# Kernel tuning notes

Measured on AMD Instinct MI355X. Metric: run time of the kernel, lower is better.

## Reference

```python
import jax, jax.numpy as jnp
import numpy as np

HEADS = 4
DIM_HEAD = 32
DIM = 512
HIDDEN = HEADS * DIM_HEAD  # 128


def setup_inputs() -> dict:
    key = jax.random.key(0)
    k1, k2, k3, k4 = jax.random.split(key, 4)
    b, l = 8, 8192
    x = jax.random.normal(k1, (b, DIM, l), dtype=jnp.float32)
    # Conv1d kernel_size=1 weights stored as [out_ch, in_ch] (squeeze kernel dim)
    w_qkv = jax.random.normal(k2, (HIDDEN * 3, DIM), dtype=jnp.float32) * (1.0 / np.sqrt(DIM))
    w_out = jax.random.normal(k3, (DIM, HIDDEN), dtype=jnp.float32) * (1.0 / np.sqrt(HIDDEN))
    b_out = jax.random.normal(k4, (DIM,), dtype=jnp.float32) * 0.01
    return {"x": x, "w_qkv": w_qkv, "w_out": w_out, "b_out": b_out}


def reference(x, w_qkv, w_out, b_out):
    b, c, l = x.shape
    # 1x1 conv == channel matmul: [b, 3*hidden, l]
    qkv = jnp.einsum('oc,bcl->bol', w_qkv, x)
    # split into q, k, v each [b, heads, dim_head, l]
    qkv = qkv.reshape(b, 3, HEADS, DIM_HEAD, l)
    q, k, v = qkv[:, 0], qkv[:, 1], qkv[:, 2]
    k = jax.nn.softmax(k, axis=-1)  # softmax over sequence positions
    # context: [b, h, d, e] (small dim_head x dim_head per head)
    context = jnp.einsum('bhdn,bhen->bhde', k, v)
    out = jnp.einsum('bhde,bhdn->bhen', context, q)  # [b, h, e, l]
    out = out.reshape(b, HIDDEN, l)
    return jnp.einsum('oc,bcl->bol', w_out, out) + b_out[None, :, None]
```

## Files before the change

### kernel.cpp

```cpp
#include <hip/hip_runtime.h>
#include <math.h>
#include <stdint.h>


#define L_LEN 8192L
#define DIMC 512

typedef short bf16x8 __attribute__((ext_vector_type(8)));
typedef float f32x4 __attribute__((ext_vector_type(4)));

__device__ __forceinline__ unsigned short f2bf(float f) {
    uint32_t u = __float_as_uint(f);
    u += 0x7FFFu + ((u >> 16) & 1u);
    return (unsigned short)(u >> 16);
}
__device__ __forceinline__ void unpack8(uint4 u, float* f) {
    f[0] = __uint_as_float(u.x << 16); f[1] = __uint_as_float(u.x & 0xFFFF0000u);
    f[2] = __uint_as_float(u.y << 16); f[3] = __uint_as_float(u.y & 0xFFFF0000u);
    f[4] = __uint_as_float(u.z << 16); f[5] = __uint_as_float(u.z & 0xFFFF0000u);
    f[6] = __uint_as_float(u.w << 16); f[7] = __uint_as_float(u.w & 0xFFFF0000u);
}

#define GLOAD_LDS16(g, l) __builtin_amdgcn_global_load_lds( \
    (const __attribute__((address_space(1))) uint32_t*)(g), \
    (__attribute__((address_space(3))) uint32_t*)(l), 16, 0, 0)

__global__ __launch_bounds__(256)
void misc_kernel(const float* __restrict__ w, unsigned short* __restrict__ wb,
                 float* __restrict__ zbase)
{
    int idx = blockIdx.x * 256 + threadIdx.x;
    if (idx < 196608) wb[idx] = f2bf(w[idx]);
    else {
        int z = idx - 196608;
        if (z < 33792) zbase[z] = 0.0f;
    }
}

__global__ __launch_bounds__(256)
void xpose_cvt_kernel(const float* __restrict__ x, unsigned short* __restrict__ xb)
{
    const int b  = blockIdx.z;
    const int c0 = blockIdx.y * 64;
    const int l0 = blockIdx.x * 64;
    const float* xp = x + (long)b * DIMC * L_LEN;
    unsigned short* op = xb + (long)b * L_LEN * DIMC;
    __shared__ float tile[64][65];
    const int t = threadIdx.x;
    #pragma unroll
    for (int r = 0; r < 4; ++r) {
        int idx = t + 256 * r;
        int row = idx >> 4, col4 = (idx & 15) * 4;
        float4 v = *(const float4*)&xp[(long)(c0 + row) * L_LEN + l0 + col4];
        tile[row][col4 + 0] = v.x;
        tile[row][col4 + 1] = v.y;
        tile[row][col4 + 2] = v.z;
        tile[row][col4 + 3] = v.w;
    }
    __syncthreads();
    #pragma unroll
    for (int r = 0; r < 4; ++r) {
        int idx = t + 256 * r;
        int lr = idx >> 4, c4 = (idx & 15) * 4;
        ushort4 o;
        o.x = f2bf(tile[c4 + 0][lr]);
        o.y = f2bf(tile[c4 + 1][lr]);
        o.z = f2bf(tile[c4 + 2][lr]);
        o.w = f2bf(tile[c4 + 3][lr]);
        *(ushort4*)&op[(long)(l0 + lr) * DIMC + c0 + c4] = o;
    }
}

template<int OUT_BF16, int KD, int FUSE_QT>
__global__ __launch_bounds__(256)
void mfma_gemm_kernel(const unsigned short* __restrict__ A, long aBS,
                      const unsigned short* __restrict__ B, long bBS,
                      void* __restrict__ Cv, long cBS,
                      const float* __restrict__ bias)
{
    const int b  = blockIdx.z;
    const int m0 = blockIdx.y * 128;
    const int l0 = blockIdx.x * 128;
    A += (long)b * aBS;
    B += (long)b * bBS;

    __shared__ unsigned short SMEM[16384];
    unsigned short* Asm = SMEM;
    unsigned short* Bsm = SMEM + 8192;

    const int t = threadIdx.x;
    const int wave = t >> 6, lane = t & 63;
    const int wm = (wave & 1) * 64, wn = (wave >> 1) * 64;
    const int srow  = wave * 16 + (lane >> 2);
    const int skoff = (lane & 3) * 8;
    const int fr = lane & 15, quad = lane >> 4;

    f32x4 acc[4][4] = {};

    for (int k0 = 0; k0 < KD; k0 += 64) {
        #pragma unroll
        for (int c = 0; c < 2; ++c) {
            const int kk = k0 + c * 32 + skoff;
            GLOAD_LDS16(A + (long)(m0 + srow) * KD + kk,      Asm + c * 4096 + wave * 512);
            GLOAD_LDS16(A + (long)(m0 + 64 + srow) * KD + kk, Asm + c * 4096 + 2048 + wave * 512);
            GLOAD_LDS16(B + (long)(l0 + srow) * KD + kk,      Bsm + c * 4096 + wave * 512);
            GLOAD_LDS16(B + (long)(l0 + 64 + srow) * KD + kk, Bsm + c * 4096 + 2048 + wave * 512);
        }
        __syncthreads();

        #pragma unroll
        for (int c = 0; c < 2; ++c) {
            bf16x8 af[4], bf[4];
            #pragma unroll
            for (int i = 0; i < 4; ++i)
                af[i] = *(const bf16x8*)&Asm[c * 4096 + (wm + i * 16 + fr) * 32 + quad * 8];
            #pragma unroll
            for (int j = 0; j < 4; ++j)
                bf[j] = *(const bf16x8*)&Bsm[c * 4096 + (wn + j * 16 + fr) * 32 + quad * 8];
            #pragma unroll
            for (int i = 0; i < 4; ++i)
                #pragma unroll
                for (int j = 0; j < 4; ++j)
                    acc[i][j] = __builtin_amdgcn_mfma_f32_16x16x32_bf16(bf[j], af[i], acc[i][j], 0, 0, 0);
        }
        __syncthreads();
    }

    if (FUSE_QT && m0 == 0) {
        #pragma unroll
        for (int i = 0; i < 4; ++i)
            #pragma unroll
            for (int j = 0; j < 4; ++j)
                #pragma unroll
                for (int r = 0; r < 4; ++r)
                    SMEM[(wn + j * 16 + quad * 4 + r) * 128 + wm + i * 16 + fr] =
                        f2bf(acc[i][j][r]);
        __syncthreads();
        unsigned short* qT = (unsigned short*)Cv + (long)b * cBS;
        #pragma unroll
        for (int rep = 0; rep < 8; ++rep) {
            int idx = rep * 256 + t;
            int row = idx >> 4, c8 = (idx & 15) * 8;
            *(uint4*)&qT[(long)(l0 + row) * 128 + c8] = *(const uint4*)&SMEM[row * 128 + c8];
        }
    } else {
        #pragma unroll
        for (int i = 0; i < 4; ++i) {
            const int m = m0 + wm + i * 16 + fr;
            const float bv = bias ? bias[m] : 0.0f;
            #pragma unroll
            for (int j = 0; j < 4; ++j) {
                const long lbase = l0 + wn + j * 16 + quad * 4;
                float v0 = acc[i][j][0] + bv, v1 = acc[i][j][1] + bv;
                float v2 = acc[i][j][2] + bv, v3 = acc[i][j][3] + bv;
                if (OUT_BF16) {
                    ushort4 o; o.x = f2bf(v0); o.y = f2bf(v1); o.z = f2bf(v2); o.w = f2bf(v3);
                    *(ushort4*)&((unsigned short*)Cv)[(long)b * cBS + (long)m * L_LEN + lbase] = o;
                } else {
                    float4 o; o.x = v0; o.y = v1; o.z = v2; o.w = v3;
                    *(float4*)&((float*)Cv)[(long)b * cBS + (long)m * L_LEN + lbase] = o;
                }
            }
        }
    }
}

__global__ __launch_bounds__(256)
void ctx_kernel(const unsigned short* __restrict__ kv, long batchStride, long kOff, long vOff,
                float* __restrict__ ctxU, float* __restrict__ S)
{
    const int bid  = blockIdx.x;
    const int esel = bid & 1;
    const int nc   = (bid >> 1) & 3;
    const int dg   = (bid >> 3) & 7;
    const int h    = (bid >> 6) & 3;
    const int b    = bid >> 8;
    const int d0   = dg * 4, e0 = esel * 16;
    const int t = threadIdx.x;
    const long n = (long)nc * 2048 + t * 8;

    const unsigned short* kp = kv + (long)b * batchStride + kOff + (long)(h * 32 + d0) * L_LEN + n;
    const unsigned short* vp = kv + (long)b * batchStride + vOff + (long)(h * 32 + e0) * L_LEN + n;

    float w8[4][8], s4[4];
    #pragma unroll
    for (int i = 0; i < 4; ++i) {
        uint4 u = *(const uint4*)&kp[(long)i * L_LEN];
        float f[8]; unpack8(u, f);
        float s = 0.0f;
        #pragma unroll
        for (int k = 0; k < 8; ++k) { w8[i][k] = __expf(f[k]); s += w8[i][k]; }
        s4[i] = s;
    }
    float acc[4][16];
    #pragma unroll
    for (int e = 0; e < 16; ++e) {
        uint4 u = *(const uint4*)&vp[(long)e * L_LEN];
        float g[8]; unpack8(u, g);
        #pragma unroll
        for (int i = 0; i < 4; ++i) {
            float s = 0.0f;
            #pragma unroll
            for (int k = 0; k < 8; ++k) s = fmaf(w8[i][k], g[k], s);
            acc[i][e] = s;
        }
    }

    const int wave = t >> 6, lane = t & 63;
    __shared__ float red[4][68];
    #pragma unroll
    for (int i = 0; i < 4; ++i) {
        #pragma unroll
        for (int e = 0; e < 16; ++e) {
            float v = acc[i][e];
            for (int off = 32; off; off >>= 1) v += __shfl_down(v, off, 64);
            if (lane == 0) red[wave][i * 16 + e] = v;
        }
        float sv = s4[i];
        for (int off = 32; off; off >>= 1) sv += __shfl_down(sv, off, 64);
        if (lane == 0) red[wave][64 + i] = sv;
    }
    __syncthreads();
    if (t < 68) {
        float v = red[0][t] + red[1][t] + red[2][t] + red[3][t];
        if (t < 64) {
            int i = t >> 4, e = t & 15;
            atomicAdd(&ctxU[(((long)(b * 4 + h) * 32) + d0 + i) * 32 + e0 + e], v);
        } else if (esel == 0) {
            atomicAdd(&S[b * 128 + h * 32 + d0 + (t - 64)], v);
        }
    }
}

template<int OUT_BF16>
__global__ __launch_bounds__(256)
void w2_kernel(const float* __restrict__ w_out, const float* __restrict__ ctxU,
               const float* __restrict__ S, void* __restrict__ out)
{
    const int idx = blockIdx.x * 256 + threadIdx.x;
    const int b = idx >> 16;
    const int rem = idx & 65535;
    const int o = rem >> 7, hd = rem & 127;
    const int h = hd >> 5, d = hd & 31;
    const float* wp = w_out + o * 128 + h * 32;
    const float* cp = ctxU + (((long)(b * 4 + h) * 32) + d) * 32;
    float s = 0.0f;
    #pragma unroll
    for (int e = 0; e < 32; e += 4) {
        float4 wv = *(const float4*)&wp[e];
        float4 cv = *(const float4*)&cp[e];
        s += wv.x * cv.x + wv.y * cv.y + wv.z * cv.z + wv.w * cv.w;
    }
    s /= S[b * 128 + hd];
    if (OUT_BF16) ((unsigned short*)out)[idx] = f2bf(s);
    else          ((float*)out)[idx] = s;
}

__global__ __launch_bounds__(256)
void weff_kernel(const float* __restrict__ W2, const float* __restrict__ wq,
                 unsigned short* __restrict__ Weffb)
{
    const int b  = blockIdx.z;
    const int ot = blockIdx.y * 64;
    const int ct = blockIdx.x * 64;
    __shared__ float W2t[64][129];
    __shared__ float wqt[128][64];
    const int t = threadIdx.x;
    const float* W2b = W2 + (long)b * 512 * 128;
    #pragma unroll
    for (int r = 0; r < 8; ++r) {
        int f4 = t + 256 * r;
        int row = f4 >> 5, c4 = (f4 & 31) * 4;
        float4 v = *(const float4*)&W2b[(long)(ot + row) * 128 + c4];
        W2t[row][c4 + 0] = v.x; W2t[row][c4 + 1] = v.y;
        W2t[row][c4 + 2] = v.z; W2t[row][c4 + 3] = v.w;
    }
    #pragma unroll
    for (int r = 0; r < 8; ++r) {
        int f4 = t + 256 * r;
        int hd = f4 >> 4, c4 = (f4 & 15) * 4;
        *(float4*)&wqt[hd][c4] = *(const float4*)&wq[(long)hd * DIMC + ct + c4];
    }
    __syncthreads();
    const int oo = (t >> 4) * 4, cc = (t & 15) * 4;
    float acc[4][4] = {};
    for (int hd = 0; hd < 128; ++hd) {
        float a[4], bb[4];
        #pragma unroll
        for (int e = 0; e < 4; ++e) a[e]  = W2t[oo + e][hd];
        #pragma unroll
        for (int e = 0; e < 4; ++e) bb[e] = wqt[hd][cc + e];
        #pragma unroll
        for (int i = 0; i < 4; ++i)
            #pragma unroll
            for (int j = 0; j < 4; ++j)
                acc[i][j] = fmaf(a[i], bb[j], acc[i][j]);
    }
    #pragma unroll
    for (int i = 0; i < 4; ++i)
        #pragma unroll
        for (int j = 0; j < 4; ++j)
            Weffb[((long)b * 512 + ot + oo + i) * 512 + ct + cc + j] = f2bf(acc[i][j]);
}

extern "C" void kernel_launch(void* const* d_in, const int* in_sizes, int n_in,
                              void* d_out, int out_size, void* d_ws, size_t ws_size,
                              hipStream_t stream)
{
    const float* x     = (const float*)d_in[0];
    const float* w_qkv = (const float*)d_in[1];
    const float* w_out = (const float*)d_in[2];
    const float* b_out = (const float*)d_in[3];
    float* out = (float*)d_out;

    char* ws = (char*)d_ws;
    unsigned short* xb = (unsigned short*)ws;

    const bool qpath = (ws_size >= 117968896UL);

    if (qpath) {
        unsigned short* qkvb = (unsigned short*)(ws + 67108864L);
        char* T = ws + 117440512L;
        unsigned short* wb = (unsigned short*)T;
        float* ctxU = (float*)(T + 393216L);
        float* Ssum = (float*)(T + 524288L);
        unsigned short* W2b = xb;

        misc_kernel<<<900, 256, 0, stream>>>(w_qkv, wb, ctxU);
        xpose_cvt_kernel<<<dim3(128, 8, 8), 256, 0, stream>>>(x, xb);
        mfma_gemm_kernel<1, 512, 1><<<dim3(64, 3, 8), 256, 0, stream>>>(
            wb, 0L, xb, L_LEN * DIMC, qkvb, 384L * L_LEN, nullptr);
        ctx_kernel<<<2048, 256, 0, stream>>>(qkvb, 384L * L_LEN, 128L * L_LEN, 256L * L_LEN,
                                             ctxU, Ssum);
        w2_kernel<1><<<2048, 256, 0, stream>>>(w_out, ctxU, Ssum, W2b);
        mfma_gemm_kernel<0, 128, 0><<<dim3(64, 4, 8), 256, 0, stream>>>(
            W2b, 512L * 128, qkvb, 384L * L_LEN, out, 512L * L_LEN, b_out);
    } else {
        unsigned short* kvb = (unsigned short*)(ws + 67108864L);
        char* T = ws + 100663296L;
        unsigned short* wb = (unsigned short*)T;
        float* ctxU = (float*)(T + 393216L);
        float* Ssum = (float*)(T + 524288L);
        unsigned short* Weffb = kvb;
        float* W2f = (float*)(ws + 67108864L + 4194304L);

        misc_kernel<<<900, 256, 0, stream>>>(w_qkv, wb, ctxU);
        xpose_cvt_kernel<<<dim3(128, 8, 8), 256, 0, stream>>>(x, xb);
        mfma_gemm_kernel<1, 512, 0><<<dim3(64, 2, 8), 256, 0, stream>>>(
            wb + 128 * DIMC, 0L, xb, L_LEN * DIMC, kvb, 256L * L_LEN, nullptr);
        ctx_kernel<<<2048, 256, 0, stream>>>(kvb, 256L * L_LEN, 0L, 128L * L_LEN,
                                             ctxU, Ssum);
        w2_kernel<0><<<2048, 256, 0, stream>>>(w_out, ctxU, Ssum, W2f);
        weff_kernel<<<dim3(8, 8, 8), 256, 0, stream>>>(W2f, w_qkv, Weffb);
        mfma_gemm_kernel<0, 512, 0><<<dim3(64, 4, 8), 256, 0, stream>>>(
            Weffb, 512L * DIMC, xb, L_LEN * DIMC, out, 512L * L_LEN, b_out);
    }
}
```

Before: 362.1 us.

## Fuse fp32-to-bf16 transpose of x into QKV GEMM B-tile load

In the main path, the separate transpose/convert kernel is dropped. The QKV GEMM now reads fp32 x directly, converts pairs of channels to packed bf16 in registers and writes them into a swizzled LDS layout. This removes one full-tensor read/write round trip of x (64MB in, 64MB bf16 out, then read back). The cost is that the B tile is loaded through registers instead of async global-to-LDS, and x is reread once per M tile (3 times).

```diff
diff --git a/kernel.cpp b/kernel.cpp
--- a/kernel.cpp
+++ b/kernel.cpp
@@ -71,10 +71,10 @@
     }
 }
 
-template<int OUT_BF16, int KD, int FUSE_QT>
+template<int OUT_BF16, int KD, int FUSE_QT, int BXF32>
 __global__ __launch_bounds__(256)
 void mfma_gemm_kernel(const unsigned short* __restrict__ A, long aBS,
-                      const unsigned short* __restrict__ B, long bBS,
+                      const void* __restrict__ Bv, long bBS,
                       void* __restrict__ Cv, long cBS,
                       const float* __restrict__ bias)
 {
@@ -82,7 +82,6 @@
     const int m0 = blockIdx.y * 128;
     const int l0 = blockIdx.x * 128;
     A += (long)b * aBS;
-    B += (long)b * bBS;
 
     __shared__ unsigned short SMEM[16384];
     unsigned short* Asm = SMEM;
@@ -94,29 +93,65 @@
     const int srow  = wave * 16 + (lane >> 2);
     const int skoff = (lane & 3) * 8;
     const int fr = lane & 15, quad = lane >> 4;
+    const int p  = t & 31;
+    const int lc = (t >> 5) * 16;
 
     f32x4 acc[4][4] = {};
 
     for (int k0 = 0; k0 < KD; k0 += 64) {
-        #pragma unroll
-        for (int c = 0; c < 2; ++c) {
-            const int kk = k0 + c * 32 + skoff;
-            GLOAD_LDS16(A + (long)(m0 + srow) * KD + kk,      Asm + c * 4096 + wave * 512);
-            GLOAD_LDS16(A + (long)(m0 + 64 + srow) * KD + kk, Asm + c * 4096 + 2048 + wave * 512);
-            GLOAD_LDS16(B + (long)(l0 + srow) * KD + kk,      Bsm + c * 4096 + wave * 512);
-            GLOAD_LDS16(B + (long)(l0 + 64 + srow) * KD + kk, Bsm + c * 4096 + 2048 + wave * 512);
+        if (BXF32) {
+            #pragma unroll
+            for (int c = 0; c < 2; ++c) {
+                const int kk = k0 + c * 32 + skoff;
+                GLOAD_LDS16(A + (long)(m0 + srow) * KD + kk,      Asm + c * 4096 + wave * 512);
+                GLOAD_LDS16(A + (long)(m0 + 64 + srow) * KD + kk, Asm + c * 4096 + 2048 + wave * 512);
+            }
+            const float* X = (const float*)Bv + (long)b * bBS;
+            const float* r0 = X + (long)(k0 + 2 * p) * L_LEN + l0 + lc;
+            const float* r1 = r0 + L_LEN;
+            float ev[16], ov[16];
+            *(float4*)&ev[0]  = *(const float4*)&r0[0];
+            *(float4*)&ev[4]  = *(const float4*)&r0[4];
+            *(float4*)&ev[8]  = *(const float4*)&r0[8];
+            *(float4*)&ev[12] = *(const float4*)&r0[12];
+            *(float4*)&ov[0]  = *(const float4*)&r1[0];
+            *(float4*)&ov[4]  = *(const float4*)&r1[4];
+            *(float4*)&ov[8]  = *(const float4*)&r1[8];
+            *(float4*)&ov[12] = *(const float4*)&r1[12];
+            uint32_t* Bw = (uint32_t*)Bsm;
+            #pragma unroll
+            for (int j = 0; j < 16; ++j) {
+                uint32_t pk = (uint32_t)f2bf(ev[j]) | ((uint32_t)f2bf(ov[j]) << 16);
+                int l = lc + j;
+                Bw[l * 32 + (p ^ ((l & 7) << 2))] = pk;
+            }
+        } else {
+            const unsigned short* B = (const unsigned short*)Bv + (long)b * bBS;
+            #pragma unroll
+            for (int c = 0; c < 2; ++c) {
+                const int kk = k0 + c * 32 + skoff;
+                GLOAD_LDS16(A + (long)(m0 + srow) * KD + kk,      Asm + c * 4096 + wave * 512);
+                GLOAD_LDS16(A + (long)(m0 + 64 + srow) * KD + kk, Asm + c * 4096 + 2048 + wave * 512);
+                GLOAD_LDS16(B + (long)(l0 + srow) * KD + kk,      Bsm + c * 4096 + wave * 512);
+                GLOAD_LDS16(B + (long)(l0 + 64 + srow) * KD + kk, Bsm + c * 4096 + 2048 + wave * 512);
+            }
         }
         __syncthreads();
 
         #pragma unroll
-        for (int c = 0; c < 2; ++c) {
+        for (int cc = 0; cc < 2; ++cc) {
             bf16x8 af[4], bf[4];
             #pragma unroll
             for (int i = 0; i < 4; ++i)
-                af[i] = *(const bf16x8*)&Asm[c * 4096 + (wm + i * 16 + fr) * 32 + quad * 8];
-            #pragma unroll
-            for (int j = 0; j < 4; ++j)
-                bf[j] = *(const bf16x8*)&Bsm[c * 4096 + (wn + j * 16 + fr) * 32 + quad * 8];
+                af[i] = *(const bf16x8*)&Asm[cc * 4096 + (wm + i * 16 + fr) * 32 + quad * 8];
+            #pragma unroll
+            for (int j = 0; j < 4; ++j) {
+                if (BXF32)
+                    bf[j] = *(const bf16x8*)&Bsm[(wn + j * 16 + fr) * 64 +
+                                                 (((cc * 4 + quad) ^ (fr & 7)) << 3)];
+                else
+                    bf[j] = *(const bf16x8*)&Bsm[cc * 4096 + (wn + j * 16 + fr) * 32 + quad * 8];
+            }
             #pragma unroll
             for (int i = 0; i < 4; ++i)
                 #pragma unroll
@@ -314,7 +349,6 @@
     float* out = (float*)d_out;
 
     char* ws = (char*)d_ws;
-    unsigned short* xb = (unsigned short*)ws;
 
     const bool qpath = (ws_size >= 117968896UL);
 
@@ -324,18 +358,18 @@
         unsigned short* wb = (unsigned short*)T;
         float* ctxU = (float*)(T + 393216L);
         float* Ssum = (float*)(T + 524288L);
-        unsigned short* W2b = xb;
+        unsigned short* W2b = (unsigned short*)ws;
 
         misc_kernel<<<900, 256, 0, stream>>>(w_qkv, wb, ctxU);
-        xpose_cvt_kernel<<<dim3(128, 8, 8), 256, 0, stream>>>(x, xb);
-        mfma_gemm_kernel<1, 512, 1><<<dim3(64, 3, 8), 256, 0, stream>>>(
-            wb, 0L, xb, L_LEN * DIMC, qkvb, 384L * L_LEN, nullptr);
+        mfma_gemm_kernel<1, 512, 1, 1><<<dim3(64, 3, 8), 256, 0, stream>>>(
+            wb, 0L, x, 512L * L_LEN, qkvb, 384L * L_LEN, nullptr);
         ctx_kernel<<<2048, 256, 0, stream>>>(qkvb, 384L * L_LEN, 128L * L_LEN, 256L * L_LEN,
                                              ctxU, Ssum);
         w2_kernel<1><<<2048, 256, 0, stream>>>(w_out, ctxU, Ssum, W2b);
-        mfma_gemm_kernel<0, 128, 0><<<dim3(64, 4, 8), 256, 0, stream>>>(
+        mfma_gemm_kernel<0, 128, 0, 0><<<dim3(64, 4, 8), 256, 0, stream>>>(
             W2b, 512L * 128, qkvb, 384L * L_LEN, out, 512L * L_LEN, b_out);
     } else {
+        unsigned short* xb = (unsigned short*)ws;
         unsigned short* kvb = (unsigned short*)(ws + 67108864L);
         char* T = ws + 100663296L;
         unsigned short* wb = (unsigned short*)T;
@@ -346,13 +380,13 @@
 
         misc_kernel<<<900, 256, 0, stream>>>(w_qkv, wb, ctxU);
         xpose_cvt_kernel<<<dim3(128, 8, 8), 256, 0, stream>>>(x, xb);
-        mfma_gemm_kernel<1, 512, 0><<<dim3(64, 2, 8), 256, 0, stream>>>(
+        mfma_gemm_kernel<1, 512, 0, 0><<<dim3(64, 2, 8), 256, 0, stream>>>(
             wb + 128 * DIMC, 0L, xb, L_LEN * DIMC, kvb, 256L * L_LEN, nullptr);
         ctx_kernel<<<2048, 256, 0, stream>>>(kvb, 256L * L_LEN, 0L, 128L * L_LEN,
                                              ctxU, Ssum);
         w2_kernel<0><<<2048, 256, 0, stream>>>(w_out, ctxU, Ssum, W2f);
         weff_kernel<<<dim3(8, 8, 8), 256, 0, stream>>>(W2f, w_qkv, Weffb);
-        mfma_gemm_kernel<0, 512, 0><<<dim3(64, 4, 8), 256, 0, stream>>>(
+        mfma_gemm_kernel<0, 512, 0, 0><<<dim3(64, 4, 8), 256, 0, stream>>>(
             Weffb, 512L * DIMC, xb, L_LEN * DIMC, out, 512L * L_LEN, b_out);
     }
 }
```

Result: no change. 355.2 us (-1.9%).

## Fuse x transpose/bf16 conversion into QKV GEMM and double-buffer GEMM LDS tiles

Applied to the files above, without the earlier changes.

The QKV GEMM now reads fp32 x directly, converts it to bf16 in registers, and writes it into a swizzled LDS layout. This removes the separate transpose/convert kernel and the round trip of xb through memory on the qpath. The GEMM main loop is also double-buffered: the next tile's A loads and B register loads are issued before the current tile's MFMA phase, which is meant to overlap memory with compute. In exchange, LDS use doubles to 64KB per block, register pressure rises, and the blocks in the three row-tiles each re-read x in fp32.

```diff
diff --git a/kernel.cpp b/kernel.cpp
--- a/kernel.cpp
+++ b/kernel.cpp
@@ -71,10 +71,10 @@
     }
 }
 
-template<int OUT_BF16, int KD, int FUSE_QT>
+template<int OUT_BF16, int KD, int FUSE_QT, int BXF32>
 __global__ __launch_bounds__(256)
 void mfma_gemm_kernel(const unsigned short* __restrict__ A, long aBS,
-                      const unsigned short* __restrict__ B, long bBS,
+                      const void* __restrict__ Bv, long bBS,
                       void* __restrict__ Cv, long cBS,
                       const float* __restrict__ bias)
 {
@@ -82,11 +82,10 @@
     const int m0 = blockIdx.y * 128;
     const int l0 = blockIdx.x * 128;
     A += (long)b * aBS;
-    B += (long)b * bBS;
-
-    __shared__ unsigned short SMEM[16384];
-    unsigned short* Asm = SMEM;
-    unsigned short* Bsm = SMEM + 8192;
+
+    __shared__ unsigned short SMEM[32768];
+    unsigned short* const Asm = SMEM;
+    unsigned short* const Bsm = SMEM + 16384;
 
     const int t = threadIdx.x;
     const int wave = t >> 6, lane = t & 63;
@@ -94,37 +93,120 @@
     const int srow  = wave * 16 + (lane >> 2);
     const int skoff = (lane & 3) * 8;
     const int fr = lane & 15, quad = lane >> 4;
-
+    const int p  = t & 31;
+    const int lc = (t >> 5) * 16;
+
+    const float* X = BXF32 ? ((const float*)Bv + (long)b * bBS) : (const float*)0;
+    const unsigned short* B16 = BXF32 ? (const unsigned short*)0
+                                      : ((const unsigned short*)Bv + (long)b * bBS);
+
+    float ev[16], ov[16];
     f32x4 acc[4][4] = {};
-
-    for (int k0 = 0; k0 < KD; k0 += 64) {
-        #pragma unroll
-        for (int c = 0; c < 2; ++c) {
-            const int kk = k0 + c * 32 + skoff;
-            GLOAD_LDS16(A + (long)(m0 + srow) * KD + kk,      Asm + c * 4096 + wave * 512);
-            GLOAD_LDS16(A + (long)(m0 + 64 + srow) * KD + kk, Asm + c * 4096 + 2048 + wave * 512);
-            GLOAD_LDS16(B + (long)(l0 + srow) * KD + kk,      Bsm + c * 4096 + wave * 512);
-            GLOAD_LDS16(B + (long)(l0 + 64 + srow) * KD + kk, Bsm + c * 4096 + 2048 + wave * 512);
-        }
+    constexpr int NT = KD / 64;
+
+#define STAGE_B_ISSUE(K0) do { \
+    const float* r0_ = X + (long)((K0) + 2 * p) * L_LEN + l0 + lc; \
+    const float* r1_ = r0_ + L_LEN; \
+    *(float4*)&ev[0]  = *(const float4*)&r0_[0]; \
+    *(float4*)&ev[4]  = *(const float4*)&r0_[4]; \
+    *(float4*)&ev[8]  = *(const float4*)&r0_[8]; \
+    *(float4*)&ev[12] = *(const float4*)&r0_[12]; \
+    *(float4*)&ov[0]  = *(const float4*)&r1_[0]; \
+    *(float4*)&ov[4]  = *(const float4*)&r1_[4]; \
+    *(float4*)&ov[8]  = *(const float4*)&r1_[8]; \
+    *(float4*)&ov[12] = *(const float4*)&r1_[12]; \
+} while (0)
+
+#define PACK_B(BUF) do { \
+    uint32_t* Bw_ = (uint32_t*)(Bsm + (BUF) * 8192); \
+    _Pragma("unroll") \
+    for (int j_ = 0; j_ < 16; ++j_) { \
+        uint32_t pk_ = (uint32_t)f2bf(ev[j_]) | ((uint32_t)f2bf(ov[j_]) << 16); \
+        int l_ = lc + j_; \
+        Bw_[l_ * 32 + (p ^ ((l_ & 7) << 2))] = pk_;   \
+    } \
+} while (0)
+
+#define STAGE_A_ISSUE(K0, BUF) do { \
+    _Pragma("unroll") \
+    for (int c_ = 0; c_ < 2; ++c_) { \
+        const int kk_ = (K0) + c_ * 32 + skoff; \
+        GLOAD_LDS16(A + (long)(m0 + srow) * KD + kk_, \
+                    Asm + (BUF) * 8192 + c_ * 4096 + wave * 512); \
+        GLOAD_LDS16(A + (long)(m0 + 64 + srow) * KD + kk_, \
+                    Asm + (BUF) * 8192 + c_ * 4096 + 2048 + wave * 512); \
+    } \
+} while (0)
+
+#define STAGE_B16_ISSUE(K0, BUF) do { \
+    _Pragma("unroll") \
+    for (int c_ = 0; c_ < 2; ++c_) { \
+        const int kk_ = (K0) + c_ * 32 + skoff; \
+        GLOAD_LDS16(B16 + (long)(l0 + srow) * KD + kk_, \
+                    Bsm + (BUF) * 8192 + c_ * 4096 + wave * 512); \
+        GLOAD_LDS16(B16 + (long)(l0 + 64 + srow) * KD + kk_, \
+                    Bsm + (BUF) * 8192 + c_ * 4096 + 2048 + wave * 512); \
+    } \
+} while (0)
+
+#define MFMA_PHASE(BUF) do { \
+    const unsigned short* Ab_ = Asm + (BUF) * 8192; \
+    const unsigned short* Bb_ = Bsm + (BUF) * 8192; \
+    _Pragma("unroll") \
+    for (int cc = 0; cc < 2; ++cc) { \
+        bf16x8 af[4], bfr[4]; \
+        _Pragma("unroll") \
+        for (int i = 0; i < 4; ++i) \
+            af[i] = *(const bf16x8*)&Ab_[cc * 4096 + (wm + i * 16 + fr) * 32 + quad * 8]; \
+        _Pragma("unroll") \
+        for (int j = 0; j < 4; ++j) { \
+            if (BXF32) \
+                bfr[j] = *(const bf16x8*)&Bb_[(wn + j * 16 + fr) * 64 + \
+                                              (((cc * 4 + quad) ^ (fr & 7)) << 3)]; \
+            else \
+                bfr[j] = *(const bf16x8*)&Bb_[cc * 4096 + (wn + j * 16 + fr) * 32 + quad * 8]; \
+        } \
+        _Pragma("unroll") \
+        for (int i = 0; i < 4; ++i) \
+            _Pragma("unroll") \
+            for (int j = 0; j < 4; ++j) \
+                acc[i][j] = __builtin_amdgcn_mfma_f32_16x16x32_bf16(bfr[j], af[i], acc[i][j], 0, 0, 0); \
+    } \
+} while (0)
+
+    if (BXF32) {
+        STAGE_B_ISSUE(0);
+        STAGE_A_ISSUE(0, 0);
+        PACK_B(0);
+    } else {
+        STAGE_A_ISSUE(0, 0);
+        STAGE_B16_ISSUE(0, 0);
+    }
+    __syncthreads();
+
+    int cur = 0;
+    #pragma unroll
+    for (int kt = 0; kt < NT; ++kt) {
+        if (kt + 1 < NT) {
+            if (BXF32) {
+                STAGE_B_ISSUE((kt + 1) * 64);
+                STAGE_A_ISSUE((kt + 1) * 64, cur ^ 1);
+            } else {
+                STAGE_A_ISSUE((kt + 1) * 64, cur ^ 1);
+                STAGE_B16_ISSUE((kt + 1) * 64, cur ^ 1);
+            }
+        }
+        MFMA_PHASE(cur);
+        if (BXF32 && kt + 1 < NT) PACK_B(cur ^ 1);
         __syncthreads();
-
-        #pragma unroll
-        for (int c = 0; c < 2; ++c) {
-            bf16x8 af[4], bf[4];
-            #pragma unroll
-            for (int i = 0; i < 4; ++i)
-                af[i] = *(const bf16x8*)&Asm[c * 4096 + (wm + i * 16 + fr) * 32 + quad * 8];
-            #pragma unroll
-            for (int j = 0; j < 4; ++j)
-                bf[j] = *(const bf16x8*)&Bsm[c * 4096 + (wn + j * 16 + fr) * 32 + quad * 8];
-            #pragma unroll
-            for (int i = 0; i < 4; ++i)
-                #pragma unroll
-                for (int j = 0; j < 4; ++j)
-                    acc[i][j] = __builtin_amdgcn_mfma_f32_16x16x32_bf16(bf[j], af[i], acc[i][j], 0, 0, 0);
-        }
-        __syncthreads();
-    }
+        cur ^= 1;
+    }
+
+#undef STAGE_B_ISSUE
+#undef PACK_B
+#undef STAGE_A_ISSUE
+#undef STAGE_B16_ISSUE
+#undef MFMA_PHASE
 
     if (FUSE_QT && m0 == 0) {
         #pragma unroll
@@ -314,7 +396,6 @@
     float* out = (float*)d_out;
 
     char* ws = (char*)d_ws;
-    unsigned short* xb = (unsigned short*)ws;
 
     const bool qpath = (ws_size >= 117968896UL);
 
@@ -324,18 +405,18 @@
         unsigned short* wb = (unsigned short*)T;
         float* ctxU = (float*)(T + 393216L);
         float* Ssum = (float*)(T + 524288L);
-        unsigned short* W2b = xb;
+        unsigned short* W2b = (unsigned short*)ws;
 
         misc_kernel<<<900, 256, 0, stream>>>(w_qkv, wb, ctxU);
-        xpose_cvt_kernel<<<dim3(128, 8, 8), 256, 0, stream>>>(x, xb);
-        mfma_gemm_kernel<1, 512, 1><<<dim3(64, 3, 8), 256, 0, stream>>>(
-            wb, 0L, xb, L_LEN * DIMC, qkvb, 384L * L_LEN, nullptr);
+        mfma_gemm_kernel<1, 512, 1, 1><<<dim3(64, 3, 8), 256, 0, stream>>>(
+            wb, 0L, x, 512L * L_LEN, qkvb, 384L * L_LEN, nullptr);
         ctx_kernel<<<2048, 256, 0, stream>>>(qkvb, 384L * L_LEN, 128L * L_LEN, 256L * L_LEN,
                                              ctxU, Ssum);
         w2_kernel<1><<<2048, 256, 0, stream>>>(w_out, ctxU, Ssum, W2b);
-        mfma_gemm_kernel<0, 128, 0><<<dim3(64, 4, 8), 256, 0, stream>>>(
+        mfma_gemm_kernel<0, 128, 0, 0><<<dim3(64, 4, 8), 256, 0, stream>>>(
             W2b, 512L * 128, qkvb, 384L * L_LEN, out, 512L * L_LEN, b_out);
     } else {
+        unsigned short* xb = (unsigned short*)ws;
         unsigned short* kvb = (unsigned short*)(ws + 67108864L);
         char* T = ws + 100663296L;
         unsigned short* wb = (unsigned short*)T;
@@ -346,13 +427,13 @@
 
         misc_kernel<<<900, 256, 0, stream>>>(w_qkv, wb, ctxU);
         xpose_cvt_kernel<<<dim3(128, 8, 8), 256, 0, stream>>>(x, xb);
-        mfma_gemm_kernel<1, 512, 0><<<dim3(64, 2, 8), 256, 0, stream>>>(
+        mfma_gemm_kernel<1, 512, 0, 0><<<dim3(64, 2, 8), 256, 0, stream>>>(
             wb + 128 * DIMC, 0L, xb, L_LEN * DIMC, kvb, 256L * L_LEN, nullptr);
         ctx_kernel<<<2048, 256, 0, stream>>>(kvb, 256L * L_LEN, 0L, 128L * L_LEN,
                                              ctxU, Ssum);
         w2_kernel<0><<<2048, 256, 0, stream>>>(w_out, ctxU, Ssum, W2f);
         weff_kernel<<<dim3(8, 8, 8), 256, 0, stream>>>(W2f, w_qkv, Weffb);
-        mfma_gemm_kernel<0, 512, 0><<<dim3(64, 4, 8), 256, 0, stream>>>(
+        mfma_gemm_kernel<0, 512, 0, 0><<<dim3(64, 4, 8), 256, 0, stream>>>(
             Weffb, 512L * DIMC, xb, L_LEN * DIMC, out, 512L * L_LEN, b_out);
     }
 }
```

After: 357.3 us. About the same (-1.3%).
